# Kernel optimization log

Hardware: AMD Instinct MI355X
Metric: run time of the kernel (lower is better)

The kernel has to match this reference:

```python
import jax, jax.numpy as jnp
import numpy as np

EPS = 0.001  # additive floor applied after relu, as in the torch code


def setup_inputs() -> dict:
    key = jax.random.key(0)
    kA, kB, kW = jax.random.split(key, 3)
    M, N, C, H, W = 512, 64, 128, 8, 8
    A = jax.random.normal(kA, (M, C, H, W), dtype=jnp.float32)
    B = jax.random.normal(kB, (N, C, H, W), dtype=jnp.float32)
    Wg = jax.random.normal(kW, (C, C), dtype=jnp.float32) * 0.01  # Wg.data.normal_(0.0, 0.01)
    return {"A": A, "B": B, "Wg": Wg}


def reference(A, B, Wg):
    # Faithful vectorization of MIMOcom.get_source_dst_max(A, B, dir=True).
    # Torch loops i,j over HxW: B0 = B[:, i, j, :]; G = B0 @ Wg;
    # combination[m, n, p] = sum_c A[m, p, c] * G[n, c]; running max over (i, j).
    M, C, H, W = A.shape
    N = B.shape[0]
    P = H * W
    Af = jnp.transpose(A, (0, 2, 3, 1)).reshape(M, P, C)  # [M, P, C]
    Bf = jnp.transpose(B, (0, 2, 3, 1)).reshape(N, P, C)  # [N, Q, C]
    G = Bf @ Wg                                           # [N, Q, D]
    scores = jnp.einsum('mpd,nqd->mnpq', Af, G)           # [M, N, P, Q]
    comb_max = scores.max(axis=-1)                        # max over B positions q
    return jax.nn.relu(comb_max) + EPS                    # [M, N, P]
```

## Files before the change

kernel.cpp:

```cpp
#include <hip/hip_runtime.h>
#include <hip/hip_bf16.h>
#include <stdint.h>

typedef __attribute__((ext_vector_type(8))) short bf16x8;
typedef __attribute__((ext_vector_type(4))) float f32x4;
using bf16 = __hip_bfloat16;

static constexpr int Mdim = 512;
static constexpr int Ndim = 64;
static constexpr int Cdim = 128;
static constexpr int Pdim = 64;
static constexpr float EPS_ADD = 0.001f;

#define SB0 __builtin_amdgcn_sched_barrier(0)
#define WAITV(N) asm volatile("s_waitcnt vmcnt(" #N ")" ::: "memory")

__device__ __forceinline__ void gll16(const void* gsrc, void* ldst) {
    const __attribute__((address_space(1))) unsigned int* g =
        (const __attribute__((address_space(1))) unsigned int*)gsrc;
    __attribute__((address_space(3))) unsigned int* l =
        (__attribute__((address_space(3))) unsigned int*)(uintptr_t)ldst;
    __builtin_amdgcn_global_load_lds(g, l, 16, 0, 0);
}

__global__ void prep_kernel(const float* __restrict__ A, const float* __restrict__ B,
                            const float* __restrict__ Wg,
                            bf16* __restrict__ Abf, bf16* __restrict__ Gbf) {
    __shared__ float lds[128 * 65];
    const int t = threadIdx.x;

    if (blockIdx.x < 512) {
        const int m = blockIdx.x;
        const float* __restrict__ Am = A + (size_t)m * (Cdim * Pdim);
#pragma unroll
        for (int i = 0; i < 8; ++i) {
            int v = t + i * 256;
            int gidx = v * 4;
            int c = gidx >> 6, p = gidx & 63;
            float4 val = *reinterpret_cast<const float4*>(Am + gidx);
            float* dst = &lds[c * 65 + p];
            dst[0] = val.x; dst[1] = val.y; dst[2] = val.z; dst[3] = val.w;
        }
        __syncthreads();

        bf16* __restrict__ dstm = Abf + (size_t)m * (Pdim * Cdim);
#pragma unroll
        for (int i = 0; i < 16; ++i) {
            int pr = t + i * 256;
            int p = pr >> 6;
            int c = (pr & 63) << 1;
            float f0 = lds[c * 65 + p];
            float f1 = lds[(c + 1) * 65 + p];
            union { bf16 h[2]; unsigned u; } pk;
            pk.h[0] = __float2bfloat16(f0);
            pk.h[1] = __float2bfloat16(f1);
            *reinterpret_cast<unsigned*>(dstm + p * Cdim + c) = pk.u;
        }
    } else {
        const int nb = blockIdx.x - 512;
        const int n  = nb >> 2;
        const int q0 = (nb & 3) * 16;
        const float* __restrict__ Bn = B + (size_t)n * (Cdim * Pdim);
#pragma unroll
        for (int i = 0; i < 8; ++i) {
            int v = t + i * 256;
            int gidx = v * 4;
            int c = gidx >> 6, q = gidx & 63;
            float4 val = *reinterpret_cast<const float4*>(Bn + gidx);
            float* dst = &lds[c * 65 + q];
            dst[0] = val.x; dst[1] = val.y; dst[2] = val.z; dst[3] = val.w;
        }
        __syncthreads();

        const int d  = t & 127;
        const int qb = q0 + (t >> 7) * 8;
        float acc[8] = {0.f, 0.f, 0.f, 0.f, 0.f, 0.f, 0.f, 0.f};
        for (int c = 0; c < 128; ++c) {
            float w = Wg[c * 128 + d];
#pragma unroll
            for (int qi = 0; qi < 8; ++qi)
                acc[qi] = fmaf(lds[c * 65 + qb + qi], w, acc[qi]);
        }
#pragma unroll
        for (int qi = 0; qi < 8; ++qi)
            Gbf[(size_t)(n * 64 + qb + qi) * Cdim + d] = __float2bfloat16(acc[qi]);
    }
}

__global__ __launch_bounds__(256, 3)
void gemm_max_kernel(const bf16* __restrict__ Abf, const bf16* __restrict__ Gbf,
                     float* __restrict__ out) {
    __shared__ bf16 sA[3][64 * 128];
    const int tid  = threadIdx.x;
    const int lane = tid & 63;
    const int w    = tid >> 6;
    const int nw = w >> 1, h = w & 1;
    const int rr = lane & 15, g = lane >> 4;
    const int bm = blockIdx.x & 15;
    const int bn = blockIdx.x >> 4;

    const bf16* Gp = Gbf + ((size_t)((bn * 2 + nw) * 64 + rr)) * 128 + g * 8;
    bf16x8 gf[4][4];
#pragma unroll
    for (int qt = 0; qt < 4; ++qt)
#pragma unroll
        for (int ks = 0; ks < 4; ++ks)
            gf[qt][ks] = *reinterpret_cast<const bf16x8*>(Gp + qt * 16 * 128 + ks * 32);
    asm volatile("" ::: "memory");

    const char* Abase = (const char*)Abf + (size_t)bm * 32 * 16384;
    auto stageA = [&](int s) {
        char* dst = (char*)&sA[s % 3][0];
        const char* src = Abase + (size_t)s * 16384;
#pragma unroll
        for (int i = 0; i < 4; ++i) {
            int f = (i * 256 + tid) * 16;
            int row = f >> 8;
            int inner = (f & 255) ^ ((row & 7) << 4);
            gll16(src + row * 256 + inner, dst + f);
        }
    };
    stageA(0);
    stageA(1);
    WAITV(8);

    f32x4 acc[4][2];

    auto compute = [&](int s) {
        const char* ab = (const char*)&sA[s % 3][0] + (h * 32 + rr) * 256;
#pragma unroll
        for (int ks = 0; ks < 4; ++ks) {
            const int off = (ks * 64 + g * 16) ^ ((rr & 7) << 4);
            bf16x8 a0 = *reinterpret_cast<const bf16x8*>(ab + off);
            bf16x8 a1 = *reinterpret_cast<const bf16x8*>(ab + 16 * 256 + off);
#pragma unroll
            for (int qt = 0; qt < 4; ++qt) {
                acc[qt][0] = __builtin_amdgcn_mfma_f32_16x16x32_bf16(
                    gf[qt][ks], a0, ks == 0 ? (f32x4){0.f,0.f,0.f,0.f} : acc[qt][0], 0, 0, 0);
                acc[qt][1] = __builtin_amdgcn_mfma_f32_16x16x32_bf16(
                    gf[qt][ks], a1, ks == 0 ? (f32x4){0.f,0.f,0.f,0.f} : acc[qt][1], 0, 0, 0);
            }
        }
    };

    auto epilogue = [&](int s) {
        float* ob = out + (size_t)(bm * 32 + s) * 4096 + (bn * 2 + nw) * 64 + h * 32;
#pragma unroll
        for (int pt = 0; pt < 2; ++pt) {
            float v = acc[0][pt][0];
#pragma unroll
            for (int qt = 0; qt < 4; ++qt)
#pragma unroll
                for (int j = 0; j < 4; ++j)
                    if (qt || j) v = fmaxf(v, acc[qt][pt][j]);
            v = fmaxf(v, __shfl_xor(v, 16));
            v = fmaxf(v, __shfl_xor(v, 32));
            if (g == 0) ob[pt * 16 + rr] = fmaxf(v, 0.f) + EPS_ADD;
        }
    };

    WAITV(4); __builtin_amdgcn_s_barrier(); SB0;
    compute(0); SB0; stageA(2); epilogue(0); SB0;

    WAITV(6); __builtin_amdgcn_s_barrier(); SB0;
    compute(1); SB0; stageA(3); epilogue(1); SB0;

    for (int s = 2; s <= 29; ++s) {
        WAITV(8); __builtin_amdgcn_s_barrier(); SB0;
        compute(s); SB0; stageA(s + 2); epilogue(s); SB0;
    }

    WAITV(8); __builtin_amdgcn_s_barrier(); SB0;
    compute(30); epilogue(30); SB0;

    WAITV(4); __builtin_amdgcn_s_barrier(); SB0;
    compute(31); epilogue(31);
}

extern "C" void kernel_launch(void* const* d_in, const int* in_sizes, int n_in,
                              void* d_out, int out_size, void* d_ws, size_t ws_size,
                              hipStream_t stream) {
    const float* A  = (const float*)d_in[0];
    const float* B  = (const float*)d_in[1];
    const float* Wg = (const float*)d_in[2];
    float* out = (float*)d_out;

    bf16* Abf = (bf16*)d_ws;
    bf16* Gbf = (bf16*)((char*)d_ws + (size_t)Mdim * Pdim * Cdim * sizeof(bf16));

    prep_kernel<<<768, 256, 0, stream>>>(A, B, Wg, Abf, Gbf);
    gemm_max_kernel<<<512, 256, 0, stream>>>(Abf, Gbf, out);
}
```

Before: 53.69 us.

## Switch GEMM-max to 32x32x16 MFMA with double buffering and finer M split

Replaces the 16x16x32 bf16 MFMA tiles with 32x32x16 tiles, so each wave holds two 32-wide accumulators and the max over q reduces with a single cross-lane shuffle. The A staging drops from a triple to a double buffer, each block now handles 16 m rows instead of 32, and the grid doubles to 1024 blocks. This aims to cut LDS reads and shuffle overhead per output and to raise parallelism. In exchange the prefetch depth is shallower, the launch-bounds occupancy target falls from 3 to 2 blocks, and G fragments are reloaded by twice as many blocks.

```diff
diff --git a/kernel.cpp b/kernel.cpp
--- a/kernel.cpp
+++ b/kernel.cpp
@@ -4,6 +4,7 @@
 
 typedef __attribute__((ext_vector_type(8))) short bf16x8;
 typedef __attribute__((ext_vector_type(4))) float f32x4;
+typedef __attribute__((ext_vector_type(16))) float f32x16;
 using bf16 = __hip_bfloat16;
 
 static constexpr int Mdim = 512;
@@ -87,30 +88,22 @@
     }
 }
 
-__global__ __launch_bounds__(256, 3)
+__global__ __launch_bounds__(256, 2)
 void gemm_max_kernel(const bf16* __restrict__ Abf, const bf16* __restrict__ Gbf,
                      float* __restrict__ out) {
-    __shared__ bf16 sA[3][64 * 128];
+    __shared__ bf16 sA[2][64 * 128];
     const int tid  = threadIdx.x;
     const int lane = tid & 63;
     const int w    = tid >> 6;
     const int nw = w >> 1, h = w & 1;
-    const int rr = lane & 15, g = lane >> 4;
-    const int bm = blockIdx.x & 15;
-    const int bn = blockIdx.x >> 4;
+    const int l31 = lane & 31, hi = lane >> 5;
+    const int mg = blockIdx.x & 31;
+    const int bn = blockIdx.x >> 5;
+    const int n  = bn * 2 + nw;
 
-    const bf16* Gp = Gbf + ((size_t)((bn * 2 + nw) * 64 + rr)) * 128 + g * 8;
-    bf16x8 gf[4][4];
-#pragma unroll
-    for (int qt = 0; qt < 4; ++qt)
-#pragma unroll
-        for (int ks = 0; ks < 4; ++ks)
-            gf[qt][ks] = *reinterpret_cast<const bf16x8*>(Gp + qt * 16 * 128 + ks * 32);
-    asm volatile("" ::: "memory");
-
-    const char* Abase = (const char*)Abf + (size_t)bm * 32 * 16384;
+    const char* Abase = (const char*)Abf + (size_t)mg * 16 * 16384;
     auto stageA = [&](int s) {
-        char* dst = (char*)&sA[s % 3][0];
+        char* dst = (char*)&sA[s & 1][0];
         const char* src = Abase + (size_t)s * 16384;
 #pragma unroll
         for (int i = 0; i < 4; ++i) {
@@ -121,60 +114,55 @@
         }
     };
     stageA(0);
-    stageA(1);
-    WAITV(8);
 
-    f32x4 acc[4][2];
+    bf16x8 gf[2][8];
+    {
+        const bf16* Gp = Gbf + ((size_t)n * 64 + l31) * 128 + hi * 8;
+#pragma unroll
+        for (int qt = 0; qt < 2; ++qt)
+#pragma unroll
+            for (int ks = 0; ks < 8; ++ks)
+                gf[qt][ks] = *reinterpret_cast<const bf16x8*>(Gp + qt * 32 * 128 + ks * 16);
+    }
+
+    f32x16 acc[2];
+    const f32x16 z16 = {0.f,0.f,0.f,0.f,0.f,0.f,0.f,0.f,0.f,0.f,0.f,0.f,0.f,0.f,0.f,0.f};
 
     auto compute = [&](int s) {
-        const char* ab = (const char*)&sA[s % 3][0] + (h * 32 + rr) * 256;
+        const char* ab = (const char*)&sA[s & 1][0] + (h * 32 + l31) * 256;
 #pragma unroll
-        for (int ks = 0; ks < 4; ++ks) {
-            const int off = (ks * 64 + g * 16) ^ ((rr & 7) << 4);
-            bf16x8 a0 = *reinterpret_cast<const bf16x8*>(ab + off);
-            bf16x8 a1 = *reinterpret_cast<const bf16x8*>(ab + 16 * 256 + off);
-#pragma unroll
-            for (int qt = 0; qt < 4; ++qt) {
-                acc[qt][0] = __builtin_amdgcn_mfma_f32_16x16x32_bf16(
-                    gf[qt][ks], a0, ks == 0 ? (f32x4){0.f,0.f,0.f,0.f} : acc[qt][0], 0, 0, 0);
-                acc[qt][1] = __builtin_amdgcn_mfma_f32_16x16x32_bf16(
-                    gf[qt][ks], a1, ks == 0 ? (f32x4){0.f,0.f,0.f,0.f} : acc[qt][1], 0, 0, 0);
-            }
+        for (int ks = 0; ks < 8; ++ks) {
+            const int off = (ks * 32 + hi * 16) ^ ((l31 & 7) << 4);
+            bf16x8 a = *reinterpret_cast<const bf16x8*>(ab + off);
+            acc[0] = __builtin_amdgcn_mfma_f32_32x32x16_bf16(
+                gf[0][ks], a, ks == 0 ? z16 : acc[0], 0, 0, 0);
+            acc[1] = __builtin_amdgcn_mfma_f32_32x32x16_bf16(
+                gf[1][ks], a, ks == 0 ? z16 : acc[1], 0, 0, 0);
         }
     };
 
     auto epilogue = [&](int s) {
-        float* ob = out + (size_t)(bm * 32 + s) * 4096 + (bn * 2 + nw) * 64 + h * 32;
+        float v = acc[0][0];
 #pragma unroll
-        for (int pt = 0; pt < 2; ++pt) {
-            float v = acc[0][pt][0];
+        for (int j = 1; j < 16; ++j) v = fmaxf(v, acc[0][j]);
 #pragma unroll
-            for (int qt = 0; qt < 4; ++qt)
-#pragma unroll
-                for (int j = 0; j < 4; ++j)
-                    if (qt || j) v = fmaxf(v, acc[qt][pt][j]);
-            v = fmaxf(v, __shfl_xor(v, 16));
-            v = fmaxf(v, __shfl_xor(v, 32));
-            if (g == 0) ob[pt * 16 + rr] = fmaxf(v, 0.f) + EPS_ADD;
-        }
+        for (int j = 0; j < 16; ++j) v = fmaxf(v, acc[1][j]);
+        v = fmaxf(v, __shfl_xor(v, 32));
+        if (hi == 0)
+            out[(size_t)(mg * 16 + s) * 4096 + n * 64 + h * 32 + l31] =
+                fmaxf(v, 0.f) + EPS_ADD;
     };
 
-    WAITV(4); __builtin_amdgcn_s_barrier(); SB0;
-    compute(0); SB0; stageA(2); epilogue(0); SB0;
+    WAITV(16); __builtin_amdgcn_s_barrier(); SB0;
+    compute(0); SB0; stageA(1); epilogue(0); SB0;
 
-    WAITV(6); __builtin_amdgcn_s_barrier(); SB0;
-    compute(1); SB0; stageA(3); epilogue(1); SB0;
-
-    for (int s = 2; s <= 29; ++s) {
-        WAITV(8); __builtin_amdgcn_s_barrier(); SB0;
-        compute(s); SB0; stageA(s + 2); epilogue(s); SB0;
+    for (int s = 1; s <= 14; ++s) {
+        WAITV(1); __builtin_amdgcn_s_barrier(); SB0;
+        compute(s); SB0; stageA(s + 1); epilogue(s); SB0;
     }
 
-    WAITV(8); __builtin_amdgcn_s_barrier(); SB0;
-    compute(30); epilogue(30); SB0;
-
-    WAITV(4); __builtin_amdgcn_s_barrier(); SB0;
-    compute(31); epilogue(31);
+    WAITV(1); __builtin_amdgcn_s_barrier(); SB0;
+    compute(15); epilogue(15);
 }
 
 extern "C" void kernel_launch(void* const* d_in, const int* in_sizes, int n_in,
@@ -189,5 +177,5 @@
     bf16* Gbf = (bf16*)((char*)d_ws + (size_t)Mdim * Pdim * Cdim * sizeof(bf16));
 
     prep_kernel<<<768, 256, 0, stream>>>(A, B, Wg, Abf, Gbf);
-    gemm_max_kernel<<<512, 256, 0, stream>>>(Abf, Gbf, out);
+    gemm_max_kernel<<<1024, 256, 0, stream>>>(Abf, Gbf, out);
 }
```

After: 52.80 us. Within noise of the previous version (-1.7%).
